# Kernel tuning notes

Measured on AMD Instinct MI355X. Metric: run time of the kernel, lower is better.

The kernel has to match this reference:

```python
import jax, jax.numpy as jnp
import numpy as np
import math

B, Hdim, Wdim, C = 8, 64, 64, 512
T, TXT = 77, 512
NH, HD = 8, 64  # num_heads, head_dim
TOP_M = 3
CLAMP_LOGIT = 2.0
CONF_THRESH = 0.35
NEG_INF = -1e30


def _ln(x, g, b, eps=1e-5):
    mu = x.mean(-1, keepdims=True)
    var = ((x - mu) ** 2).mean(-1, keepdims=True)
    return (x - mu) * jax.lax.rsqrt(var + eps) * g + b


def _l2norm(x, eps=1e-6):
    n = jnp.sqrt((x * x).sum(-1, keepdims=True))
    return x / jnp.maximum(n, eps)


def setup_inputs() -> dict:
    key = jax.random.key(0)
    ks = jax.random.split(key, 16)
    s = 0.02
    inp = {
        'visual_features': jax.random.normal(ks[0], (B, Hdim, Wdim, C), jnp.float32),
        'text_features': jax.random.normal(ks[1], (B, T, TXT), jnp.float32),
        'ln1_g': jnp.ones((C,), jnp.float32), 'ln1_b': jnp.zeros((C,), jnp.float32),
        'ln2_g': jnp.ones((C,), jnp.float32), 'ln2_b': jnp.zeros((C,), jnp.float32),
        'Wq': jax.random.normal(ks[2], (C, C), jnp.float32) * s, 'bq': jnp.zeros((C,), jnp.float32),
        'Wk': jax.random.normal(ks[3], (TXT, C), jnp.float32) * s, 'bk': jnp.zeros((C,), jnp.float32),
        'Wv': jax.random.normal(ks[4], (TXT, C), jnp.float32) * s, 'bv': jnp.zeros((C,), jnp.float32),
        'Wo': jax.random.normal(ks[5], (C, C), jnp.float32) * s, 'bo': jnp.zeros((C,), jnp.float32),
        'Wg': jax.random.normal(ks[6], (C, 1), jnp.float32) * s, 'bg': jnp.zeros((1,), jnp.float32),
        'W1': jax.random.normal(ks[7], (C, 4 * C), jnp.float32) * s, 'b1': jnp.zeros((4 * C,), jnp.float32),
        'W2': jax.random.normal(ks[8], (4 * C, C), jnp.float32) * s, 'b2': jnp.zeros((C,), jnp.float32),
        'logit_scale': jnp.asarray(math.log(1.0 / 0.07), jnp.float32),
        'alpha': jnp.asarray(0.1, jnp.float32),
    }
    return inp


def reference(visual_features, text_features, ln1_g, ln1_b, ln2_g, ln2_b,
              Wq, bq, Wk, bk, Wv, bv, Wo, bo, Wg, bg, W1, b1, W2, b2,
              logit_scale, alpha):
    b, h, w, c = visual_features.shape
    n = h * w
    # Pre-LN on visual tokens
    x = _ln(visual_features, ln1_g, ln1_b).reshape(b, n, c)
    q_full = x @ Wq + bq                                   # [B,N,C]
    pad_mask = jnp.abs(text_features).sum(-1) <= 1e-6      # [B,T]
    k_full = text_features @ Wk + bk                       # [B,T,C]
    v_full = text_features @ Wv + bv
    # l2-normalize over full channel dim, then split heads
    q = _l2norm(q_full).reshape(b, n, NH, HD)
    k = _l2norm(k_full).reshape(b, T, NH, HD)
    v = v_full.reshape(b, T, NH, HD)
    scale = jnp.exp(jnp.clip(logit_scale, -CLAMP_LOGIT, CLAMP_LOGIT)) / math.sqrt(float(HD))
    sim = jnp.einsum('bnhd,bthd->bnht', q, k) * scale      # [B,N,H,T]
    sim = jnp.where(pad_mask[:, None, None, :], NEG_INF, sim)
    # top-k sparsification: keep top_m per (b,n,h) row
    topv = jax.lax.top_k(sim, TOP_M)[0][..., -1:]
    sim = jnp.where(sim >= topv, sim, NEG_INF)
    attn = jax.nn.softmax(sim, axis=-1)
    attn = attn / jnp.maximum(attn.sum(-1, keepdims=True), 1e-6)
    all_pad = pad_mask.all(axis=1)                         # [B]
    attn = jnp.where(all_pad[:, None, None, None], 0.0, attn)
    # confidence: max-prob * (1 - normalized entropy), mean over heads
    attn_hn = attn.transpose(0, 2, 1, 3)                   # [B,H,N,T]
    maxp = attn_hn.max(-1, keepdims=True)
    t_eff = jnp.maximum((attn_hn > 0).astype(jnp.float32).sum(-1, keepdims=True), 2.0)
    p = jnp.maximum(attn_hn, 1e-8)
    entropy = jnp.maximum(-(p * jnp.log(p)).sum(-1, keepdims=True) / jnp.log(t_eff), 0.0)
    conf = jnp.clip(maxp * (1.0 - entropy), 0.0, 1.0).mean(axis=1)  # [B,N,1]
    bypass = (conf >= CONF_THRESH).astype(attn.dtype)
    aligned = jnp.einsum('bnht,bthd->bnhd', attn, v).reshape(b, n, c)
    aligned = (aligned @ Wo + bo) * bypass
    gate = jax.nn.sigmoid(x @ Wg + bg)                     # [B,N,1]
    y = x + alpha * gate * aligned
    y = _ln(y, ln2_g, ln2_b)
    y = y + (jax.nn.gelu(y @ W1 + b1, approximate=False) @ W2 + b2)
    return y.reshape(b, h, w, c)
```

## Files before the change

kernel.cpp:

```cpp
#include <hip/hip_runtime.h>
#include <stdint.h>

#define BATCH 8
#define NTOK 4096
#define CDIM 512
#define TTXT 77
#define TPAD 80
#define NHEAD 8
#define HDIM 64
#define HID 2048
#define MROWS 32768
#define NEGINF (-1e30f)

typedef __attribute__((ext_vector_type(8))) short short8;
typedef __attribute__((ext_vector_type(4))) float f32x4;

__device__ __forceinline__ float b2f(unsigned short u) {
    union { unsigned int i; float f; } x; x.i = ((unsigned int)u) << 16; return x.f;
}
__device__ __forceinline__ unsigned short f2b(float f) {
    union { float f; unsigned int i; } x; x.f = f;
    unsigned int i = x.i;
    return (unsigned short)((i + 0x7fffu + ((i >> 16) & 1u)) >> 16);
}

__device__ __forceinline__ void gload16(const void* g, void* l) {
    __builtin_amdgcn_global_load_lds(
        (const __attribute__((address_space(1))) unsigned int*)g,
        (__attribute__((address_space(3))) unsigned int*)l, 16, 0, 0);
}

#define OFF_WQT   ((size_t)0)
#define OFF_WKT   (OFF_WQT + 512*512*2)
#define OFF_WVT   (OFF_WKT + 512*512*2)
#define OFF_WOT   (OFF_WVT + 512*512*2)
#define OFF_W1T   (OFF_WOT + 512*512*2)
#define OFF_W2T   (OFF_W1T + (size_t)2048*512*2)
#define OFF_TEXTB (OFF_W2T + (size_t)512*2048*2)
#define OFF_KFB   (OFF_TEXTB + (size_t)640*512*2)
#define OFF_KNRM  (OFF_KFB + (size_t)640*512*2)
#define OFF_VPAD  (OFF_KNRM + (size_t)640*512*2)
#define OFF_PADM  (OFF_VPAD + (size_t)640*512*2)
#define OFF_ALLP  (OFF_PADM + 2560)
#define OFF_GATE  (OFF_ALLP + 256)
#define OFF_BYP   (OFF_GATE + (size_t)MROWS*4)
#define OFF_XB    (OFF_BYP + (size_t)MROWS*4)
#define OFF_BUFB  (OFF_XB + (size_t)MROWS*CDIM*2)
#define OFF_BUFC  (OFF_BUFB + (size_t)MROWS*CDIM*2)
#define OFF_H     (OFF_BUFC + (size_t)MROWS*CDIM*2)
#define WS_NEED   (OFF_H + (size_t)MROWS*HID*2)
#define OFF_VT    OFF_H

__device__ __forceinline__ float waveReduceAdd(float v) {
#pragma unroll
    for (int m = 1; m < 64; m <<= 1) v += __shfl_xor(v, m);
    return v;
}
__device__ __forceinline__ float red16Max(float v) {
#pragma unroll
    for (int m = 1; m < 16; m <<= 1) v = fmaxf(v, __shfl_xor(v, m));
    return v;
}
__device__ __forceinline__ float red16Add(float v) {
#pragma unroll
    for (int m = 1; m < 16; m <<= 1) v += __shfl_xor(v, m);
    return v;
}
__device__ __forceinline__ float red16Min(float v) {
#pragma unroll
    for (int m = 1; m < 16; m <<= 1) v = fminf(v, __shfl_xor(v, m));
    return v;
}

__global__ __launch_bounds__(256) void prep_kernel(
    const float* __restrict__ Wq, const float* __restrict__ Wk,
    const float* __restrict__ Wv, const float* __restrict__ Wo,
    const float* __restrict__ W1, const float* __restrict__ W2,
    unsigned short* __restrict__ WQT, unsigned short* __restrict__ WKT,
    unsigned short* __restrict__ WVT, unsigned short* __restrict__ WOT,
    unsigned short* __restrict__ W1T, unsigned short* __restrict__ W2T,
    const float* __restrict__ text, unsigned short* __restrict__ textb,
    float* __restrict__ padm, unsigned short* __restrict__ vt)
{
    __shared__ float tile[32][33];
    __shared__ float sred[4];
    int b = blockIdx.x;
    const int tid = threadIdx.x;

    if (b >= 3712) {
        const int i = b - 3712;
        const int bh = i * 4 + (tid >> 6), d = tid & 63;
        uint4 z = {0u, 0u, 0u, 0u};
        uint4* p = (uint4*)(vt + ((size_t)bh * 64 + d) * 96 + 80);
        p[0] = z; p[1] = z;
        return;
    }
    if (b >= 3072) {
        const int r = b - 3072;
        const int tb = r / TPAD, t = r % TPAD;
        if (t < TTXT) {
            const float2 v = ((const float2*)(text + ((size_t)(tb * TTXT + t)) * 512))[tid];
            float a = fabsf(v.x) + fabsf(v.y);
            a = waveReduceAdd(a);
            if ((tid & 63) == 0) sred[tid >> 6] = a;
            __syncthreads();
            const float asum = sred[0] + sred[1] + sred[2] + sred[3];
            ushort2 o; o.x = f2b(v.x); o.y = f2b(v.y);
            ((ushort2*)(textb + (size_t)r * 512))[tid] = o;
            if (tid == 0) padm[r] = (asum <= 1e-6f) ? 1.f : 0.f;
        } else {
            ushort2 z; z.x = 0; z.y = 0;
            ((ushort2*)(textb + (size_t)r * 512))[tid] = z;
            if (tid == 0) padm[r] = 1.f;
        }
        return;
    }

    const float* src; unsigned short* dst; int R, C, cx, ry;
    if (b < 1024)       { src = W1; dst = W1T; R = 512;  C = 2048; cx = b & 63; ry = b >> 6; }
    else if (b < 2048)  { b -= 1024; src = W2; dst = W2T; R = 2048; C = 512; cx = b & 15; ry = b >> 4; }
    else {
        b -= 2048; const int which = b >> 8; b &= 255;
        R = 512; C = 512; cx = b & 15; ry = b >> 4;
        src = (which == 0) ? Wq : (which == 1) ? Wk : (which == 2) ? Wv : Wo;
        dst = (which == 0) ? WQT : (which == 1) ? WKT : (which == 2) ? WVT : WOT;
    }
    const int tx = threadIdx.x & 31, ty = threadIdx.x >> 5;
    const int c0 = cx * 32, r0 = ry * 32;
#pragma unroll
    for (int i = 0; i < 32; i += 8)
        tile[ty + i][tx] = src[(size_t)(r0 + ty + i) * C + c0 + tx];
    __syncthreads();
#pragma unroll
    for (int i = 0; i < 32; i += 8)
        dst[(size_t)(c0 + ty + i) * R + r0 + tx] = f2b(tile[tx][ty + i]);
}

__global__ __launch_bounds__(128) void ln1_gate_kernel(
    const float* __restrict__ vin, const float* __restrict__ g1, const float* __restrict__ b1v,
    const float* __restrict__ Wg, const float* __restrict__ bg,
    unsigned short* __restrict__ xb, float* __restrict__ gate)
{
    __shared__ float sred[4];
    const int row = blockIdx.x, tid = threadIdx.x;
    const float4 v = *(const float4*)(vin + (size_t)row * 512 + tid * 4);
    float s = v.x + v.y + v.z + v.w;
    float s2 = v.x * v.x + v.y * v.y + v.z * v.z + v.w * v.w;
    s = waveReduceAdd(s); s2 = waveReduceAdd(s2);
    if ((tid & 63) == 0) { sred[tid >> 6] = s; sred[2 + (tid >> 6)] = s2; }
    __syncthreads();
    s = sred[0] + sred[1]; s2 = sred[2] + sred[3];
    const float mu = s * (1.f / 512.f);
    float var = s2 * (1.f / 512.f) - mu * mu;
    const float rs = rsqrtf(fmaxf(var, 0.f) + 1e-5f);
    const float4 gg = *(const float4*)(g1 + tid * 4);
    const float4 bb = *(const float4*)(b1v + tid * 4);
    const float x0 = (v.x - mu) * rs * gg.x + bb.x;
    const float x1 = (v.y - mu) * rs * gg.y + bb.y;
    const float x2 = (v.z - mu) * rs * gg.z + bb.z;
    const float x3 = (v.w - mu) * rs * gg.w + bb.w;
    ushort4 o; o.x = f2b(x0); o.y = f2b(x1); o.z = f2b(x2); o.w = f2b(x3);
    *(ushort4*)(xb + (size_t)row * 512 + tid * 4) = o;
    const float4 wg = *(const float4*)(Wg + tid * 4);
    float gp = x0 * wg.x + x1 * wg.y + x2 * wg.z + x3 * wg.w;
    gp = waveReduceAdd(gp);
    __syncthreads();
    if ((tid & 63) == 0) sred[tid >> 6] = gp;
    __syncthreads();
    if (tid == 0) {
        float z = sred[0] + sred[1] + bg[0];
        gate[row] = 1.f / (1.f + __expf(-z));
    }
}

__global__ __launch_bounds__(128) void ln2_kernel(
    const unsigned short* __restrict__ yin, const float* __restrict__ g2, const float* __restrict__ b2v,
    unsigned short* __restrict__ yb)
{
    __shared__ float sred[4];
    const int row = blockIdx.x, tid = threadIdx.x;
    ushort4 u = *(const ushort4*)(yin + (size_t)row * 512 + tid * 4);
    float v0 = b2f(u.x), v1 = b2f(u.y), v2 = b2f(u.z), v3 = b2f(u.w);
    float s = v0 + v1 + v2 + v3;
    float s2 = v0 * v0 + v1 * v1 + v2 * v2 + v3 * v3;
    s = waveReduceAdd(s); s2 = waveReduceAdd(s2);
    if ((tid & 63) == 0) { sred[tid >> 6] = s; sred[2 + (tid >> 6)] = s2; }
    __syncthreads();
    s = sred[0] + sred[1]; s2 = sred[2] + sred[3];
    const float mu = s * (1.f / 512.f);
    float var = s2 * (1.f / 512.f) - mu * mu;
    const float rs = rsqrtf(fmaxf(var, 0.f) + 1e-5f);
    const float4 gg = *(const float4*)(g2 + tid * 4);
    const float4 bb = *(const float4*)(b2v + tid * 4);
    ushort4 o;
    o.x = f2b((v0 - mu) * rs * gg.x + bb.x);
    o.y = f2b((v1 - mu) * rs * gg.y + bb.y);
    o.z = f2b((v2 - mu) * rs * gg.z + bb.z);
    o.w = f2b((v3 - mu) * rs * gg.w + bb.w);
    *(ushort4*)(yb + (size_t)row * 512 + tid * 4) = o;
}

__global__ __launch_bounds__(128) void l2norm_kernel(
    const unsigned short* __restrict__ in, unsigned short* __restrict__ out)
{
    __shared__ float sred[2];
    const int row = blockIdx.x, tid = threadIdx.x;
    ushort4 u = *(const ushort4*)(in + (size_t)row * 512 + tid * 4);
    float v0 = b2f(u.x), v1 = b2f(u.y), v2 = b2f(u.z), v3 = b2f(u.w);
    float ss = v0 * v0 + v1 * v1 + v2 * v2 + v3 * v3;
    ss = waveReduceAdd(ss);
    if ((tid & 63) == 0) sred[tid >> 6] = ss;
    __syncthreads();
    ss = sred[0] + sred[1];
    const float inv = 1.f / fmaxf(sqrtf(ss), 1e-6f);
    ushort4 o;
    o.x = f2b(v0 * inv); o.y = f2b(v1 * inv); o.z = f2b(v2 * inv); o.w = f2b(v3 * inv);
    *(ushort4*)(out + (size_t)row * 512 + tid * 4) = o;
}

__global__ __launch_bounds__(256) void gemm_kv(
    const unsigned short* __restrict__ A,
    const unsigned short* __restrict__ BtK, const unsigned short* __restrict__ BtV,
    const float* __restrict__ bk, const float* __restrict__ bv,
    unsigned short* __restrict__ kfb, unsigned short* __restrict__ vt)
{
    const int K = 512, N = 512;
    const unsigned short* Bt = blockIdx.z ? BtV : BtK;
    const float* bias = blockIdx.z ? bv : bk;
    __shared__ unsigned short sA[128 * 64];
    __shared__ unsigned short sB[128 * 64];
    char* cA = (char*)sA;
    char* cB = (char*)sB;
    const int tid = threadIdx.x;
    const int lane = tid & 63, w = tid >> 6;
    const int g = lane >> 4, ln = lane & 15;
    const int WR = w >> 1, WC = w & 1;
    const int rowA0 = blockIdx.x * 128, colB0 = blockIdx.y * 128;

    f32x4 acc[4][4];
#pragma unroll
    for (int m = 0; m < 4; ++m)
#pragma unroll
        for (int n = 0; n < 4; ++n) acc[m][n] = (f32x4){0.f, 0.f, 0.f, 0.f};

    for (int k0 = 0; k0 < K; k0 += 64) {
        __syncthreads();
#pragma unroll
        for (int i = 0; i < 4; ++i) {
            int c = tid + i * 256;
            int row = c >> 3, kc = c & 7;
            int kcs = kc ^ (row & 7);
            gload16(A + (size_t)(rowA0 + row) * K + k0 + kcs * 8, cA + c * 16);
            gload16(Bt + (size_t)(colB0 + row) * K + k0 + kcs * 8, cB + c * 16);
        }
        __syncthreads();
#pragma unroll
        for (int kk = 0; kk < 2; ++kk) {
            short8 af[4], bf[4];
#pragma unroll
            for (int m = 0; m < 4; ++m) {
                int row = WR * 64 + m * 16 + ln;
                af[m] = *(const short8*)(cA + row * 128 + ((kk * 64 + g * 16) ^ ((row & 7) << 4)));
            }
#pragma unroll
            for (int n = 0; n < 4; ++n) {
                int col = WC * 64 + n * 16 + ln;
                bf[n] = *(const short8*)(cB + col * 128 + ((kk * 64 + g * 16) ^ ((col & 7) << 4)));
            }
#pragma unroll
            for (int m = 0; m < 4; ++m)
#pragma unroll
                for (int n = 0; n < 4; ++n)
                    acc[m][n] = __builtin_amdgcn_mfma_f32_16x16x32_bf16(af[m], bf[n], acc[m][n], 0, 0, 0);
        }
    }

#pragma unroll
    for (int m = 0; m < 4; ++m) {
        const int rbase = rowA0 + WR * 64 + m * 16 + g * 4;
#pragma unroll
        for (int n = 0; n < 4; ++n) {
            const int col = colB0 + WC * 64 + n * 16 + ln;
            const float bcol = bias[col];
#pragma unroll
            for (int i = 0; i < 4; ++i) {
                const int row = rbase + i;
                const float v = acc[m][n][i] + bcol;
                if (blockIdx.z == 0) {
                    kfb[(size_t)row * N + col] = f2b(v);
                } else {
                    const int tb = row / TPAD, t = row - tb * TPAD;
                    const int h = col >> 6, d = col & 63;
                    vt[((size_t)(tb * NHEAD + h) * 64 + d) * 96 + t] = f2b(v);
                }
            }
        }
    }
}

#define SEAM() __builtin_amdgcn_sched_barrier(0x106)

template<int EPI>
__global__ __launch_bounds__(512, 2) void gemm256(
    const unsigned short* __restrict__ A, const unsigned short* __restrict__ Bt,
    const float* __restrict__ bias,
    unsigned short* __restrict__ outb, float* __restrict__ outf,
    int M, int N, int K,
    const unsigned short* __restrict__ xres, const float* __restrict__ gate,
    const float* __restrict__ byp, const unsigned short* __restrict__ yres,
    const float* __restrict__ alphaPtr, int gxM, int gyN)
{
    __shared__ unsigned short lds[2][2][16384];
    const int tid = threadIdx.x;
    const int lane = tid & 63, w = tid >> 6;
    const int g = lane >> 4, ln = lane & 15;
    const int wr = w >> 2, wc = w & 3;

    int bm, bn;
    {
        const int L = (int)blockIdx.x;
        const int xcd = L & 7, j = L >> 3;
        const int rl = j / gyN;
        bn = j - rl * gyN;
        bm = xcd * (gxM >> 3) + rl;
    }
    const int rowA0 = bm * 256, colB0 = bn * 256;
    const int nt = K >> 6;

    auto stageA = [&](int t, int mh) {
        const int buf = t & 1;
#pragma unroll
        for (int r = 0; r < 2; ++r) {
            const int c = tid + r * 512;
            const int prl = c >> 3, kc = c & 7;
            const int grow = rowA0 + ((prl >> 6) << 7) + (mh << 6) + (prl & 63);
            gload16(A + (size_t)grow * K + (t << 6) + ((kc ^ (prl & 7)) << 3),
                    (char*)&lds[buf][0][mh * 8192] + c * 16);
        }
    };
    auto stageB = [&](int t, int nh) {
        const int buf = t & 1;
#pragma unroll
        for (int r = 0; r < 2; ++r) {
            const int c = tid + r * 512;
            const int prl = c >> 3, kc = c & 7;
            const int gcol = colB0 + ((prl >> 5) << 6) + (nh << 5) + (prl & 31);
            gload16(Bt + (size_t)gcol * K + (t << 6) + ((kc ^ (prl & 7)) << 3),
                    (char*)&lds[buf][1][nh * 8192] + c * 16);
        }
    };

    f32x4 acc[8][4];
#pragma unroll
    for (int m = 0; m < 8; ++m)
#pragma unroll
        for (int n = 0; n < 4; ++n) acc[m][n] = (f32x4){0.f, 0.f, 0.f, 0.f};

    stageA(0, 0); stageA(0, 1); stageB(0, 0); stageB(0, 1);
    asm volatile("s_waitcnt vmcnt(0)" ::: "memory");
    __builtin_amdgcn_s_barrier();

    const int sw  = (ln & 7) << 4;
    const int kb0 = (g * 16) ^ sw;
    const int kb1 = (64 + g * 16) ^ sw;
    const int arow = (wr * 64 + ln) * 128;
    const int brow = (wc * 32 + ln) * 128;

    short8 afr[4][2], bfr[4][2];

#pragma unroll 2
    for (int t = 0; t < nt; ++t) {
        const char* lA = (const char*)&lds[t & 1][0][0];
        const char* lB = (const char*)&lds[t & 1][1][0];
        const bool pf = (t + 1 < nt);

#pragma unroll
        for (int m = 0; m < 4; ++m) {
            afr[m][0] = *(const short8*)(lA + arow + m * 2048 + kb0);
            afr[m][1] = *(const short8*)(lA + arow + m * 2048 + kb1);
        }
#pragma unroll
        for (int n = 0; n < 2; ++n) {
            bfr[n][0] = *(const short8*)(lB + brow + n * 2048 + kb0);
            bfr[n][1] = *(const short8*)(lB + brow + n * 2048 + kb1);
        }
        if (pf) { stageA(t + 1, 0); stageA(t + 1, 1); }
        __builtin_amdgcn_s_setprio(1);
#pragma unroll
        for (int m = 0; m < 4; ++m)
#pragma unroll
            for (int n = 0; n < 2; ++n) {
                acc[m][n] = __builtin_amdgcn_mfma_f32_16x16x32_bf16(afr[m][0], bfr[n][0], acc[m][n], 0, 0, 0);
                acc[m][n] = __builtin_amdgcn_mfma_f32_16x16x32_bf16(afr[m][1], bfr[n][1], acc[m][n], 0, 0, 0);
            }
        __builtin_amdgcn_s_setprio(0);
        SEAM();

#pragma unroll
        for (int n = 2; n < 4; ++n) {
            bfr[n][0] = *(const short8*)(lB + brow + (n & 1) * 2048 + 16384 + kb0);
            bfr[n][1] = *(const short8*)(lB + brow + (n & 1) * 2048 + 16384 + kb1);
        }
        if (pf) { stageB(t + 1, 0); stageB(t + 1, 1); }
        __builtin_amdgcn_s_setprio(1);
#pragma unroll
        for (int m = 0; m < 4; ++m)
#pragma unroll
            for (int n = 2; n < 4; ++n) {
                acc[m][n] = __builtin_amdgcn_mfma_f32_16x16x32_bf16(afr[m][0], bfr[n][0], acc[m][n], 0, 0, 0);
                acc[m][n] = __builtin_amdgcn_mfma_f32_16x16x32_bf16(afr[m][1], bfr[n][1], acc[m][n], 0, 0, 0);
            }
        __builtin_amdgcn_s_setprio(0);
        SEAM();

#pragma unroll
        for (int m = 0; m < 4; ++m) {
            afr[m][0] = *(const short8*)(lA + arow + m * 2048 + 16384 + kb0);
            afr[m][1] = *(const short8*)(lA + arow + m * 2048 + 16384 + kb1);
        }
        __builtin_amdgcn_s_setprio(1);
#pragma unroll
        for (int m = 0; m < 4; ++m)
#pragma unroll
            for (int n = 0; n < 2; ++n) {
                acc[m + 4][n] = __builtin_amdgcn_mfma_f32_16x16x32_bf16(afr[m][0], bfr[n][0], acc[m + 4][n], 0, 0, 0);
                acc[m + 4][n] = __builtin_amdgcn_mfma_f32_16x16x32_bf16(afr[m][1], bfr[n][1], acc[m + 4][n], 0, 0, 0);
            }
        __builtin_amdgcn_s_setprio(0);
        SEAM();

        __builtin_amdgcn_s_setprio(1);
#pragma unroll
        for (int m = 0; m < 4; ++m)
#pragma unroll
            for (int n = 2; n < 4; ++n) {
                acc[m + 4][n] = __builtin_amdgcn_mfma_f32_16x16x32_bf16(afr[m][0], bfr[n][0], acc[m + 4][n], 0, 0, 0);
                acc[m + 4][n] = __builtin_amdgcn_mfma_f32_16x16x32_bf16(afr[m][1], bfr[n][1], acc[m + 4][n], 0, 0, 0);
            }
        __builtin_amdgcn_s_setprio(0);

        if (pf) {
            asm volatile("s_waitcnt vmcnt(0)" ::: "memory");
            __builtin_amdgcn_s_barrier();
        }
    }

    const float alpha = (EPI == 1) ? *alphaPtr : 0.f;
#pragma unroll
    for (int m = 0; m < 8; ++m) {
        const int rbase = rowA0 + wr * 128 + m * 16 + g * 4;
#pragma unroll
        for (int n = 0; n < 4; ++n) {
            const int col = colB0 + wc * 64 + n * 16 + ln;
            const float bcol = bias[col];
#pragma unroll
            for (int i = 0; i < 4; ++i) {
                const int row = rbase + i;
                const float v = acc[m][n][i] + bcol;
                if (EPI == 0) {
                    outb[(size_t)row * N + col] = f2b(v);
                } else if (EPI == 1) {
                    float yp = b2f(xres[(size_t)row * N + col]) + alpha * gate[row] * byp[row] * v;
                    outb[(size_t)row * N + col] = f2b(yp);
                } else if (EPI == 2) {
                    const float u2 = 2.f * v * (0.7978845608f + 0.0356774081f * v * v);
                    const float tt = 1.f - 2.f / (__expf(u2) + 1.f);
                    outb[(size_t)row * N + col] = f2b(0.5f * v * (1.f + tt));
                } else {
                    outf[(size_t)row * N + col] = b2f(yres[(size_t)row * N + col]) + v;
                }
            }
        }
    }
}
#undef SEAM

__global__ __launch_bounds__(256) void attn_kernel(
    const unsigned short* __restrict__ qn,
    const unsigned short* __restrict__ kn,
    const unsigned short* __restrict__ vt,
    const float* __restrict__ padm,
    const float* __restrict__ lscPtr,
    unsigned short* __restrict__ aligned,
    float* __restrict__ bypass)
{
    const int b = blockIdx.y;
    const int n0 = blockIdx.x * 16;
    const int tid = threadIdx.x;
    const int w = tid >> 6, lane = tid & 63, g = lane >> 4, ln = lane & 15;
    __shared__ unsigned short s_p[4][16][104];
    __shared__ float s_conf[4][16];
    __shared__ float s_inv[16];

    float pm[5];
#pragma unroll
    for (int tt = 0; tt < 5; ++tt) {
        int t = ln + tt * 16;
        pm[tt] = (t < TTXT) ? padm[b * TPAD + t] : 1.f;
    }
    {
        float pmn = fminf(fminf(pm[0], pm[1]), fminf(fminf(pm[2], pm[3]), pm[4]));
        pmn = red16Min(pmn);
        if (pmn > 0.5f) {
            uint4 z = {0u, 0u, 0u, 0u};
#pragma unroll
            for (int j = 0; j < 4; ++j) {
                int id = tid + j * 256;
                int row = id >> 6, c8 = id & 63;
                *(uint4*)(aligned + ((size_t)(b * NTOK + n0 + row)) * 512 + c8 * 8) = z;
            }
            if (tid < 16) bypass[b * NTOK + n0 + tid] = 0.f;
            return;
        }
    }

    {
        const int r = tid >> 4, seg = tid & 15;
        const unsigned short* qp = qn + ((size_t)(b * NTOK + n0 + r)) * 512 + seg * 32;
        float ss = 0.f;
#pragma unroll
        for (int j = 0; j < 4; ++j) {
            short8 u = *(const short8*)(qp + j * 8);
#pragma unroll
            for (int e = 0; e < 8; ++e) {
                float f = b2f(((const unsigned short*)&u)[e]);
                ss += f * f;
            }
        }
        ss = red16Add(ss);
        if (seg == 0) s_inv[r] = 1.f / fmaxf(sqrtf(ss), 1e-6f);
    }

    float lscale;
    {
        float ls = *lscPtr;
        ls = fminf(fmaxf(ls, -2.f), 2.f);
        lscale = __expf(ls) * 0.125f;
    }

    for (int j = g; j < 24; j += 4) s_p[w][ln][80 + j] = 0;
    __syncthreads();

    float conf_acc[4] = {0.f, 0.f, 0.f, 0.f};
    const size_t qrow = ((size_t)(b * NTOK + n0 + ln)) * 512;

#pragma unroll
    for (int hh = 0; hh < 2; ++hh) {
        const int h = w + hh * 4;
        short8 a0 = *(const short8*)(qn + qrow + h * 64 + g * 8);
        short8 a1 = *(const short8*)(qn + qrow + h * 64 + 32 + g * 8);
        f32x4 sim[5];
#pragma unroll
        for (int tt = 0; tt < 5; ++tt) {
            const size_t kbase = ((size_t)(b * TPAD + tt * 16 + ln)) * 512 + h * 64;
            short8 b0 = *(const short8*)(kn + kbase + g * 8);
            short8 b1 = *(const short8*)(kn + kbase + 32 + g * 8);
            f32x4 c = (f32x4){0.f, 0.f, 0.f, 0.f};
            c = __builtin_amdgcn_mfma_f32_16x16x32_bf16(a0, b0, c, 0, 0, 0);
            c = __builtin_amdgcn_mfma_f32_16x16x32_bf16(a1, b1, c, 0, 0, 0);
            sim[tt] = c;
        }
#pragma unroll
        for (int i = 0; i < 4; ++i) {
            const float qs = lscale * s_inv[g * 4 + i];
            float v[5];
#pragma unroll
            for (int tt = 0; tt < 5; ++tt)
                v[tt] = (pm[tt] == 0.f) ? sim[tt][i] * qs : NEGINF;

            float lm = v[0];
#pragma unroll
            for (int tt = 1; tt < 5; ++tt) lm = fmaxf(lm, v[tt]);
            const float m1 = red16Max(lm);
            float lm2 = -3.0e38f;
#pragma unroll
            for (int tt = 0; tt < 5; ++tt) if (v[tt] < m1) lm2 = fmaxf(lm2, v[tt]);
            const float m2 = red16Max(lm2);
            float lm3 = -3.0e38f;
#pragma unroll
            for (int tt = 0; tt < 5; ++tt) if (v[tt] < m2) lm3 = fmaxf(lm3, v[tt]);
            const float m3 = red16Max(lm3);
            float lc = 0.f;
#pragma unroll
            for (int tt = 0; tt < 5; ++tt) {
                if (v[tt] >= m1) lc += 1.f;
                if (v[tt] >= m2) lc += 128.f;
            }
            const float cpk = red16Add(lc);
            const float c2 = floorf(cpk * (1.f / 128.f));
            const float c1 = cpk - 128.f * c2;
            const float th = (c1 >= 3.f) ? m1 : ((c2 >= 3.f) ? m2 : m3);

            float p[5], lsum = 0.f, lcnt = 0.f;
#pragma unroll
            for (int tt = 0; tt < 5; ++tt) {
                float pv = (v[tt] >= th) ? __expf(v[tt] - m1) : 0.f;
                p[tt] = pv;
                lsum += pv;
                lcnt += (pv > 0.f) ? 1.f : 0.f;
            }
            const float psum = red16Add(lsum);
            const float pcnt = red16Add(lcnt);
            const float inv = 1.f / fmaxf(psum, 1e-20f);

            float lmaxp = 0.f, lent = 0.f;
#pragma unroll
            for (int tt = 0; tt < 5; ++tt) {
                float a = p[tt] * inv;
                p[tt] = a;
                lmaxp = fmaxf(lmaxp, a);
                if (a > 0.f) {
                    float pp = fmaxf(a, 1e-8f);
                    lent += -pp * __logf(pp);
                }
            }
            const float maxp = red16Max(lmaxp);
            float ent = red16Add(lent);
            ent += (77.f - pcnt) * 1.8420680744e-7f;
            const float teff = fmaxf(pcnt, 2.f);
            const float entropy = fmaxf(ent / __logf(teff), 0.f);
            const float confh = fminf(fmaxf(maxp * (1.f - entropy), 0.f), 1.f);
            conf_acc[i] += confh;

#pragma unroll
            for (int tt = 0; tt < 5; ++tt)
                s_p[w][g * 4 + i][ln + tt * 16] = f2b(p[tt]);
        }
        short8 af[3];
#pragma unroll
        for (int k = 0; k < 3; ++k)
            af[k] = *(const short8*)(&s_p[w][ln][k * 32 + g * 8]);
        const size_t vtb = ((size_t)(b * NHEAD + h)) * 64;
#pragma unroll
        for (int n = 0; n < 4; ++n) {
            f32x4 o = (f32x4){0.f, 0.f, 0.f, 0.f};
#pragma unroll
            for (int k = 0; k < 3; ++k) {
                short8 bf = *(const short8*)(vt + (vtb + n * 16 + ln) * 96 + k * 32 + g * 8);
                o = __builtin_amdgcn_mfma_f32_16x16x32_bf16(af[k], bf, o, 0, 0, 0);
            }
#pragma unroll
            for (int i = 0; i < 4; ++i)
                aligned[((size_t)(b * NTOK + n0 + g * 4 + i)) * 512 + h * 64 + n * 16 + ln] =
                    f2b(o[i]);
        }
    }

    if (ln == 0) {
#pragma unroll
        for (int i = 0; i < 4; ++i) s_conf[w][g * 4 + i] = conf_acc[i];
    }
    __syncthreads();
    if (tid < 16) {
        float c = (s_conf[0][tid] + s_conf[1][tid] + s_conf[2][tid] + s_conf[3][tid]) * 0.125f;
        bypass[b * NTOK + n0 + tid] = (c >= 0.35f) ? 1.f : 0.f;
    }
}

extern "C" void kernel_launch(void* const* d_in, const int* in_sizes, int n_in,
                              void* d_out, int out_size, void* d_ws, size_t ws_size,
                              hipStream_t stream)
{
    (void)in_sizes; (void)n_in; (void)out_size;
    if (ws_size < WS_NEED) return;

    const float* visual = (const float*)d_in[0];
    const float* text   = (const float*)d_in[1];
    const float* ln1_g  = (const float*)d_in[2];
    const float* ln1_b  = (const float*)d_in[3];
    const float* ln2_g  = (const float*)d_in[4];
    const float* ln2_b  = (const float*)d_in[5];
    const float* Wq = (const float*)d_in[6];   const float* bq = (const float*)d_in[7];
    const float* Wk = (const float*)d_in[8];   const float* bk = (const float*)d_in[9];
    const float* Wv = (const float*)d_in[10];  const float* bv = (const float*)d_in[11];
    const float* Wo = (const float*)d_in[12];  const float* bo = (const float*)d_in[13];
    const float* Wg = (const float*)d_in[14];  const float* bg = (const float*)d_in[15];
    const float* W1 = (const float*)d_in[16];  const float* b1 = (const float*)d_in[17];
    const float* W2 = (const float*)d_in[18];  const float* b2 = (const float*)d_in[19];
    const float* lsc = (const float*)d_in[20];
    const float* alp = (const float*)d_in[21];

    char* ws = (char*)d_ws;
    unsigned short* WQT  = (unsigned short*)(ws + OFF_WQT);
    unsigned short* WKT  = (unsigned short*)(ws + OFF_WKT);
    unsigned short* WVT  = (unsigned short*)(ws + OFF_WVT);
    unsigned short* WOT  = (unsigned short*)(ws + OFF_WOT);
    unsigned short* W1T  = (unsigned short*)(ws + OFF_W1T);
    unsigned short* W2T  = (unsigned short*)(ws + OFF_W2T);
    unsigned short* TEXTB = (unsigned short*)(ws + OFF_TEXTB);
    unsigned short* KFB  = (unsigned short*)(ws + OFF_KFB);
    unsigned short* KNRM = (unsigned short*)(ws + OFF_KNRM);
    float* PADM = (float*)(ws + OFF_PADM);
    float* GATE = (float*)(ws + OFF_GATE);
    float* BYP  = (float*)(ws + OFF_BYP);
    unsigned short* XB   = (unsigned short*)(ws + OFF_XB);
    unsigned short* BUFB = (unsigned short*)(ws + OFF_BUFB);
    unsigned short* BUFC = (unsigned short*)(ws + OFF_BUFC);
    unsigned short* HBUF = (unsigned short*)(ws + OFF_H);
    unsigned short* VT   = (unsigned short*)(ws + OFF_VT);
    float* out = (float*)d_out;

    prep_kernel<<<3728, 256, 0, stream>>>(Wq, Wk, Wv, Wo, W1, W2,
                                          WQT, WKT, WVT, WOT, W1T, W2T,
                                          text, TEXTB, PADM, VT);

    ln1_gate_kernel<<<MROWS, 128, 0, stream>>>(visual, ln1_g, ln1_b, Wg, bg, XB, GATE);

    gemm_kv<<<dim3(5, 4, 2), 256, 0, stream>>>(TEXTB, WKT, WVT, bk, bv, KFB, VT);
    l2norm_kernel<<<640, 128, 0, stream>>>(KFB, KNRM);

    gemm256<0><<<dim3(128 * 2), 512, 0, stream>>>(XB, WQT, bq, BUFB, nullptr, MROWS, 512, 512,
                                                  nullptr, nullptr, nullptr, nullptr, nullptr,
                                                  128, 2);

    attn_kernel<<<dim3(NTOK / 16, BATCH), 256, 0, stream>>>(BUFB, KNRM, VT, PADM, lsc,
                                                            BUFC, BYP);

    gemm256<1><<<dim3(128 * 2), 512, 0, stream>>>(BUFC, WOT, bo, BUFB, nullptr, MROWS, 512, 512,
                                                  XB, GATE, BYP, nullptr, alp, 128, 2);

    ln2_kernel<<<MROWS, 128, 0, stream>>>(BUFB, ln2_g, ln2_b, XB);

    gemm256<2><<<dim3(128 * 8), 512, 0, stream>>>(XB, W1T, b1, HBUF, nullptr, MROWS, HID, 512,
                                                  nullptr, nullptr, nullptr, nullptr, nullptr,
                                                  128, 8);
    gemm256<3><<<dim3(128 * 2), 512, 0, stream>>>(HBUF, W2T, b2, nullptr, out, MROWS, 512, HID,
                                                  nullptr, nullptr, nullptr, XB, nullptr,
                                                  128, 2);
}
```

Measured before the change: 363.1 us.

## Add triple-buffered K=32 GEMM variant for the FFN matmuls

Adds a new GEMM kernel that stages 32-wide K tiles into three rotating LDS buffers with a two-tile-ahead prefetch, partial vmcnt waits, and a simpler XOR swizzle. Each iteration then issues all 32 MFMAs in one burst. The two FFN GEMMs (W1 with GELU, W2 with residual) switch to it. The epilogue is moved into a shared helper. The aim is to hide global load latency better and cut per-tile synchronisation stalls, at the cost of twice as many barriers per K and a different LDS bank access pattern.

```diff
diff --git a/kernel.cpp b/kernel.cpp
--- a/kernel.cpp
+++ b/kernel.cpp
@@ -298,153 +298,15 @@
     }
 }
 
-#define SEAM() __builtin_amdgcn_sched_barrier(0x106)
-
 template<int EPI>
-__global__ __launch_bounds__(512, 2) void gemm256(
-    const unsigned short* __restrict__ A, const unsigned short* __restrict__ Bt,
+__device__ __forceinline__ void gemm_epilogue(
+    f32x4 (&acc)[8][4], int rowA0, int colB0, int wr, int wc, int g, int ln,
     const float* __restrict__ bias,
-    unsigned short* __restrict__ outb, float* __restrict__ outf,
-    int M, int N, int K,
+    unsigned short* __restrict__ outb, float* __restrict__ outf, int N,
     const unsigned short* __restrict__ xres, const float* __restrict__ gate,
     const float* __restrict__ byp, const unsigned short* __restrict__ yres,
-    const float* __restrict__ alphaPtr, int gxM, int gyN)
-{
-    __shared__ unsigned short lds[2][2][16384];
-    const int tid = threadIdx.x;
-    const int lane = tid & 63, w = tid >> 6;
-    const int g = lane >> 4, ln = lane & 15;
-    const int wr = w >> 2, wc = w & 3;
-
-    int bm, bn;
-    {
-        const int L = (int)blockIdx.x;
-        const int xcd = L & 7, j = L >> 3;
-        const int rl = j / gyN;
-        bn = j - rl * gyN;
-        bm = xcd * (gxM >> 3) + rl;
-    }
-    const int rowA0 = bm * 256, colB0 = bn * 256;
-    const int nt = K >> 6;
-
-    auto stageA = [&](int t, int mh) {
-        const int buf = t & 1;
-#pragma unroll
-        for (int r = 0; r < 2; ++r) {
-            const int c = tid + r * 512;
-            const int prl = c >> 3, kc = c & 7;
-            const int grow = rowA0 + ((prl >> 6) << 7) + (mh << 6) + (prl & 63);
-            gload16(A + (size_t)grow * K + (t << 6) + ((kc ^ (prl & 7)) << 3),
-                    (char*)&lds[buf][0][mh * 8192] + c * 16);
-        }
-    };
-    auto stageB = [&](int t, int nh) {
-        const int buf = t & 1;
-#pragma unroll
-        for (int r = 0; r < 2; ++r) {
-            const int c = tid + r * 512;
-            const int prl = c >> 3, kc = c & 7;
-            const int gcol = colB0 + ((prl >> 5) << 6) + (nh << 5) + (prl & 31);
-            gload16(Bt + (size_t)gcol * K + (t << 6) + ((kc ^ (prl & 7)) << 3),
-                    (char*)&lds[buf][1][nh * 8192] + c * 16);
-        }
-    };
-
-    f32x4 acc[8][4];
-#pragma unroll
-    for (int m = 0; m < 8; ++m)
-#pragma unroll
-        for (int n = 0; n < 4; ++n) acc[m][n] = (f32x4){0.f, 0.f, 0.f, 0.f};
-
-    stageA(0, 0); stageA(0, 1); stageB(0, 0); stageB(0, 1);
-    asm volatile("s_waitcnt vmcnt(0)" ::: "memory");
-    __builtin_amdgcn_s_barrier();
-
-    const int sw  = (ln & 7) << 4;
-    const int kb0 = (g * 16) ^ sw;
-    const int kb1 = (64 + g * 16) ^ sw;
-    const int arow = (wr * 64 + ln) * 128;
-    const int brow = (wc * 32 + ln) * 128;
-
-    short8 afr[4][2], bfr[4][2];
-
-#pragma unroll 2
-    for (int t = 0; t < nt; ++t) {
-        const char* lA = (const char*)&lds[t & 1][0][0];
-        const char* lB = (const char*)&lds[t & 1][1][0];
-        const bool pf = (t + 1 < nt);
-
-#pragma unroll
-        for (int m = 0; m < 4; ++m) {
-            afr[m][0] = *(const short8*)(lA + arow + m * 2048 + kb0);
-            afr[m][1] = *(const short8*)(lA + arow + m * 2048 + kb1);
-        }
-#pragma unroll
-        for (int n = 0; n < 2; ++n) {
-            bfr[n][0] = *(const short8*)(lB + brow + n * 2048 + kb0);
-            bfr[n][1] = *(const short8*)(lB + brow + n * 2048 + kb1);
-        }
-        if (pf) { stageA(t + 1, 0); stageA(t + 1, 1); }
-        __builtin_amdgcn_s_setprio(1);
-#pragma unroll
-        for (int m = 0; m < 4; ++m)
-#pragma unroll
-            for (int n = 0; n < 2; ++n) {
-                acc[m][n] = __builtin_amdgcn_mfma_f32_16x16x32_bf16(afr[m][0], bfr[n][0], acc[m][n], 0, 0, 0);
-                acc[m][n] = __builtin_amdgcn_mfma_f32_16x16x32_bf16(afr[m][1], bfr[n][1], acc[m][n], 0, 0, 0);
-            }
-        __builtin_amdgcn_s_setprio(0);
-        SEAM();
-
-#pragma unroll
-        for (int n = 2; n < 4; ++n) {
-            bfr[n][0] = *(const short8*)(lB + brow + (n & 1) * 2048 + 16384 + kb0);
-            bfr[n][1] = *(const short8*)(lB + brow + (n & 1) * 2048 + 16384 + kb1);
-        }
-        if (pf) { stageB(t + 1, 0); stageB(t + 1, 1); }
-        __builtin_amdgcn_s_setprio(1);
-#pragma unroll
-        for (int m = 0; m < 4; ++m)
-#pragma unroll
-            for (int n = 2; n < 4; ++n) {
-                acc[m][n] = __builtin_amdgcn_mfma_f32_16x16x32_bf16(afr[m][0], bfr[n][0], acc[m][n], 0, 0, 0);
-                acc[m][n] = __builtin_amdgcn_mfma_f32_16x16x32_bf16(afr[m][1], bfr[n][1], acc[m][n], 0, 0, 0);
-            }
-        __builtin_amdgcn_s_setprio(0);
-        SEAM();
-
-#pragma unroll
-        for (int m = 0; m < 4; ++m) {
-            afr[m][0] = *(const short8*)(lA + arow + m * 2048 + 16384 + kb0);
-            afr[m][1] = *(const short8*)(lA + arow + m * 2048 + 16384 + kb1);
-        }
-        __builtin_amdgcn_s_setprio(1);
-#pragma unroll
-        for (int m = 0; m < 4; ++m)
-#pragma unroll
-            for (int n = 0; n < 2; ++n) {
-                acc[m + 4][n] = __builtin_amdgcn_mfma_f32_16x16x32_bf16(afr[m][0], bfr[n][0], acc[m + 4][n], 0, 0, 0);
-                acc[m + 4][n] = __builtin_amdgcn_mfma_f32_16x16x32_bf16(afr[m][1], bfr[n][1], acc[m + 4][n], 0, 0, 0);
-            }
-        __builtin_amdgcn_s_setprio(0);
-        SEAM();
-
-        __builtin_amdgcn_s_setprio(1);
-#pragma unroll
-        for (int m = 0; m < 4; ++m)
-#pragma unroll
-            for (int n = 2; n < 4; ++n) {
-                acc[m + 4][n] = __builtin_amdgcn_mfma_f32_16x16x32_bf16(afr[m][0], bfr[n][0], acc[m + 4][n], 0, 0, 0);
-                acc[m + 4][n] = __builtin_amdgcn_mfma_f32_16x16x32_bf16(afr[m][1], bfr[n][1], acc[m + 4][n], 0, 0, 0);
-            }
-        __builtin_amdgcn_s_setprio(0);
-
-        if (pf) {
-            asm volatile("s_waitcnt vmcnt(0)" ::: "memory");
-            __builtin_amdgcn_s_barrier();
-        }
-    }
-
+    const float* __restrict__ alphaPtr)
+{
     const float alpha = (EPI == 1) ? *alphaPtr : 0.f;
 #pragma unroll
     for (int m = 0; m < 8; ++m) {
@@ -473,7 +335,258 @@
         }
     }
 }
+
+#define SEAM() __builtin_amdgcn_sched_barrier(0x106)
+
+template<int EPI>
+__global__ __launch_bounds__(512, 2) void gemm256(
+    const unsigned short* __restrict__ A, const unsigned short* __restrict__ Bt,
+    const float* __restrict__ bias,
+    unsigned short* __restrict__ outb, float* __restrict__ outf,
+    int M, int N, int K,
+    const unsigned short* __restrict__ xres, const float* __restrict__ gate,
+    const float* __restrict__ byp, const unsigned short* __restrict__ yres,
+    const float* __restrict__ alphaPtr, int gxM, int gyN)
+{
+    __shared__ unsigned short lds[2][2][16384];
+    const int tid = threadIdx.x;
+    const int lane = tid & 63, w = tid >> 6;
+    const int g = lane >> 4, ln = lane & 15;
+    const int wr = w >> 2, wc = w & 3;
+
+    int bm, bn;
+    {
+        const int L = (int)blockIdx.x;
+        const int xcd = L & 7, j = L >> 3;
+        const int rl = j / gyN;
+        bn = j - rl * gyN;
+        bm = xcd * (gxM >> 3) + rl;
+    }
+    const int rowA0 = bm * 256, colB0 = bn * 256;
+    const int nt = K >> 6;
+
+    auto stageA = [&](int t, int mh) {
+        const int buf = t & 1;
+#pragma unroll
+        for (int r = 0; r < 2; ++r) {
+            const int c = tid + r * 512;
+            const int prl = c >> 3, kc = c & 7;
+            const int grow = rowA0 + ((prl >> 6) << 7) + (mh << 6) + (prl & 63);
+            gload16(A + (size_t)grow * K + (t << 6) + ((kc ^ (prl & 7)) << 3),
+                    (char*)&lds[buf][0][mh * 8192] + c * 16);
+        }
+    };
+    auto stageB = [&](int t, int nh) {
+        const int buf = t & 1;
+#pragma unroll
+        for (int r = 0; r < 2; ++r) {
+            const int c = tid + r * 512;
+            const int prl = c >> 3, kc = c & 7;
+            const int gcol = colB0 + ((prl >> 5) << 6) + (nh << 5) + (prl & 31);
+            gload16(Bt + (size_t)gcol * K + (t << 6) + ((kc ^ (prl & 7)) << 3),
+                    (char*)&lds[buf][1][nh * 8192] + c * 16);
+        }
+    };
+
+    f32x4 acc[8][4];
+#pragma unroll
+    for (int m = 0; m < 8; ++m)
+#pragma unroll
+        for (int n = 0; n < 4; ++n) acc[m][n] = (f32x4){0.f, 0.f, 0.f, 0.f};
+
+    stageA(0, 0); stageA(0, 1); stageB(0, 0); stageB(0, 1);
+    asm volatile("s_waitcnt vmcnt(0)" ::: "memory");
+    __builtin_amdgcn_s_barrier();
+
+    const int sw  = (ln & 7) << 4;
+    const int kb0 = (g * 16) ^ sw;
+    const int kb1 = (64 + g * 16) ^ sw;
+    const int arow = (wr * 64 + ln) * 128;
+    const int brow = (wc * 32 + ln) * 128;
+
+    short8 afr[4][2], bfr[4][2];
+
+#pragma unroll 2
+    for (int t = 0; t < nt; ++t) {
+        const char* lA = (const char*)&lds[t & 1][0][0];
+        const char* lB = (const char*)&lds[t & 1][1][0];
+        const bool pf = (t + 1 < nt);
+
+#pragma unroll
+        for (int m = 0; m < 4; ++m) {
+            afr[m][0] = *(const short8*)(lA + arow + m * 2048 + kb0);
+            afr[m][1] = *(const short8*)(lA + arow + m * 2048 + kb1);
+        }
+#pragma unroll
+        for (int n = 0; n < 2; ++n) {
+            bfr[n][0] = *(const short8*)(lB + brow + n * 2048 + kb0);
+            bfr[n][1] = *(const short8*)(lB + brow + n * 2048 + kb1);
+        }
+        if (pf) { stageA(t + 1, 0); stageA(t + 1, 1); }
+        __builtin_amdgcn_s_setprio(1);
+#pragma unroll
+        for (int m = 0; m < 4; ++m)
+#pragma unroll
+            for (int n = 0; n < 2; ++n) {
+                acc[m][n] = __builtin_amdgcn_mfma_f32_16x16x32_bf16(afr[m][0], bfr[n][0], acc[m][n], 0, 0, 0);
+                acc[m][n] = __builtin_amdgcn_mfma_f32_16x16x32_bf16(afr[m][1], bfr[n][1], acc[m][n], 0, 0, 0);
+            }
+        __builtin_amdgcn_s_setprio(0);
+        SEAM();
+
+#pragma unroll
+        for (int n = 2; n < 4; ++n) {
+            bfr[n][0] = *(const short8*)(lB + brow + (n & 1) * 2048 + 16384 + kb0);
+            bfr[n][1] = *(const short8*)(lB + brow + (n & 1) * 2048 + 16384 + kb1);
+        }
+        if (pf) { stageB(t + 1, 0); stageB(t + 1, 1); }
+        __builtin_amdgcn_s_setprio(1);
+#pragma unroll
+        for (int m = 0; m < 4; ++m)
+#pragma unroll
+            for (int n = 2; n < 4; ++n) {
+                acc[m][n] = __builtin_amdgcn_mfma_f32_16x16x32_bf16(afr[m][0], bfr[n][0], acc[m][n], 0, 0, 0);
+                acc[m][n] = __builtin_amdgcn_mfma_f32_16x16x32_bf16(afr[m][1], bfr[n][1], acc[m][n], 0, 0, 0);
+            }
+        __builtin_amdgcn_s_setprio(0);
+        SEAM();
+
+#pragma unroll
+        for (int m = 0; m < 4; ++m) {
+            afr[m][0] = *(const short8*)(lA + arow + m * 2048 + 16384 + kb0);
+            afr[m][1] = *(const short8*)(lA + arow + m * 2048 + 16384 + kb1);
+        }
+        __builtin_amdgcn_s_setprio(1);
+#pragma unroll
+        for (int m = 0; m < 4; ++m)
+#pragma unroll
+            for (int n = 0; n < 2; ++n) {
+                acc[m + 4][n] = __builtin_amdgcn_mfma_f32_16x16x32_bf16(afr[m][0], bfr[n][0], acc[m + 4][n], 0, 0, 0);
+                acc[m + 4][n] = __builtin_amdgcn_mfma_f32_16x16x32_bf16(afr[m][1], bfr[n][1], acc[m + 4][n], 0, 0, 0);
+            }
+        __builtin_amdgcn_s_setprio(0);
+        SEAM();
+
+        __builtin_amdgcn_s_setprio(1);
+#pragma unroll
+        for (int m = 0; m < 4; ++m)
+#pragma unroll
+            for (int n = 2; n < 4; ++n) {
+                acc[m + 4][n] = __builtin_amdgcn_mfma_f32_16x16x32_bf16(afr[m][0], bfr[n][0], acc[m + 4][n], 0, 0, 0);
+                acc[m + 4][n] = __builtin_amdgcn_mfma_f32_16x16x32_bf16(afr[m][1], bfr[n][1], acc[m + 4][n], 0, 0, 0);
+            }
+        __builtin_amdgcn_s_setprio(0);
+
+        if (pf) {
+            asm volatile("s_waitcnt vmcnt(0)" ::: "memory");
+            __builtin_amdgcn_s_barrier();
+        }
+    }
+
+    gemm_epilogue<EPI>(acc, rowA0, colB0, wr, wc, g, ln, bias, outb, outf, N,
+                       xres, gate, byp, yres, alphaPtr);
+}
 #undef SEAM
+
+template<int EPI>
+__global__ __launch_bounds__(512, 2) void gemm256t(
+    const unsigned short* __restrict__ A, const unsigned short* __restrict__ Bt,
+    const float* __restrict__ bias,
+    unsigned short* __restrict__ outb, float* __restrict__ outf,
+    int M, int N, int K,
+    const unsigned short* __restrict__ xres, const float* __restrict__ gate,
+    const float* __restrict__ byp, const unsigned short* __restrict__ yres,
+    const float* __restrict__ alphaPtr, int gxM, int gyN)
+{
+    __shared__ unsigned short lds[3][2][8192];
+    const int tid = threadIdx.x;
+    const int lane = tid & 63, w = tid >> 6;
+    const int g = lane >> 4, ln = lane & 15;
+    const int wr = w >> 2, wc = w & 3;
+
+    int bm, bn;
+    {
+        const int L = (int)blockIdx.x;
+        const int xcd = L & 7, j = L >> 3;
+        const int rl = j / gyN;
+        bn = j - rl * gyN;
+        bm = xcd * (gxM >> 3) + rl;
+    }
+    const int rowA0 = bm * 256, colB0 = bn * 256;
+    const int nt = K >> 5;
+
+    auto stageA = [&](int t, int buf) {
+#pragma unroll
+        for (int r = 0; r < 2; ++r) {
+            const int c = tid + r * 512;
+            const int row = c >> 2, kc = c & 3;
+            const int kcs = kc ^ ((row >> 1) & 3);
+            gload16(A + (size_t)(rowA0 + row) * K + (t << 5) + (kcs << 3),
+                    (char*)&lds[buf][0][0] + c * 16);
+        }
+    };
+    auto stageB = [&](int t, int buf) {
+#pragma unroll
+        for (int r = 0; r < 2; ++r) {
+            const int c = tid + r * 512;
+            const int row = c >> 2, kc = c & 3;
+            const int kcs = kc ^ ((row >> 1) & 3);
+            gload16(Bt + (size_t)(colB0 + row) * K + (t << 5) + (kcs << 3),
+                    (char*)&lds[buf][1][0] + c * 16);
+        }
+    };
+
+    f32x4 acc[8][4];
+#pragma unroll
+    for (int m = 0; m < 8; ++m)
+#pragma unroll
+        for (int n = 0; n < 4; ++n) acc[m][n] = (f32x4){0.f, 0.f, 0.f, 0.f};
+
+    stageA(0, 0); stageB(0, 0);
+    stageA(1, 1); stageB(1, 1);
+    asm volatile("s_waitcnt vmcnt(4)" ::: "memory");
+    __builtin_amdgcn_s_barrier();
+
+    const int swz = (g ^ ((ln >> 1) & 3)) << 4;
+    const int arow = (wr * 128 + ln) * 64 + swz;
+    const int brow = (wc * 64 + ln) * 64 + swz;
+
+    short8 af[8], bf[4];
+    int cb = 0;
+
+    for (int t = 0; t < nt; ++t) {
+        const char* lA = (const char*)&lds[cb][0][0];
+        const char* lB = (const char*)&lds[cb][1][0];
+
+#pragma unroll
+        for (int m = 0; m < 8; ++m) af[m] = *(const short8*)(lA + arow + m * 1024);
+#pragma unroll
+        for (int n = 0; n < 4; ++n) bf[n] = *(const short8*)(lB + brow + n * 1024);
+
+        if (t + 2 < nt) {
+            int nb = cb + 2; if (nb >= 3) nb -= 3;
+            stageA(t + 2, nb); stageB(t + 2, nb);
+        }
+
+        __builtin_amdgcn_s_setprio(1);
+#pragma unroll
+        for (int m = 0; m < 8; ++m)
+#pragma unroll
+            for (int n = 0; n < 4; ++n)
+                acc[m][n] = __builtin_amdgcn_mfma_f32_16x16x32_bf16(af[m], bf[n], acc[m][n], 0, 0, 0);
+        __builtin_amdgcn_s_setprio(0);
+
+        if (t + 1 < nt) {
+            if (t + 2 < nt) { asm volatile("s_waitcnt vmcnt(4)" ::: "memory"); }
+            else            { asm volatile("s_waitcnt vmcnt(0)" ::: "memory"); }
+            __builtin_amdgcn_s_barrier();
+        }
+        cb = (cb == 2) ? 0 : cb + 1;
+    }
+
+    gemm_epilogue<EPI>(acc, rowA0, colB0, wr, wc, g, ln, bias, outb, outf, N,
+                       xres, gate, byp, yres, alphaPtr);
+}
 
 __global__ __launch_bounds__(256) void attn_kernel(
     const unsigned short* __restrict__ qn,
@@ -721,10 +834,10 @@
 
     ln2_kernel<<<MROWS, 128, 0, stream>>>(BUFB, ln2_g, ln2_b, XB);
 
-    gemm256<2><<<dim3(128 * 8), 512, 0, stream>>>(XB, W1T, b1, HBUF, nullptr, MROWS, HID, 512,
-                                                  nullptr, nullptr, nullptr, nullptr, nullptr,
-                                                  128, 8);
-    gemm256<3><<<dim3(128 * 2), 512, 0, stream>>>(HBUF, W2T, b2, nullptr, out, MROWS, 512, HID,
-                                                  nullptr, nullptr, nullptr, XB, nullptr,
-                                                  128, 2);
-}
+    gemm256t<2><<<dim3(128 * 8), 512, 0, stream>>>(XB, W1T, b1, HBUF, nullptr, MROWS, HID, 512,
+                                                   nullptr, nullptr, nullptr, nullptr, nullptr,
+                                                   128, 8);
+    gemm256t<3><<<dim3(128 * 2), 512, 0, stream>>>(HBUF, W2T, b2, nullptr, out, MROWS, 512, HID,
+                                                   nullptr, nullptr, nullptr, XB, nullptr,
+                                                   128, 2);
+}
```

Measured after the change: 372.2 us. 2.5% more time.
